# Performance work log

Measured on AMD Instinct MI355X. Metric: run time of the kernel, lower is better.

## Reference

```python
import jax, jax.numpy as jnp
import numpy as np

N_NODES = 100000
N_EDGES = 1600000
D = 128
L = 3


def setup_inputs() -> dict:
    key = jax.random.key(0)
    k1, k2, k3 = jax.random.split(key, 3)
    edge_index = jax.random.randint(k1, (2, N_EDGES), 0, N_NODES, dtype=jnp.int64)
    emb = jax.random.normal(k2, (N_NODES, D), dtype=jnp.float32)
    # Glorot-style scale for the per-layer linear weights
    Ws = jax.random.normal(k3, (L, D, D), dtype=jnp.float32) * (1.0 / np.sqrt(D))
    bs = jnp.zeros((L, D), dtype=jnp.float32)
    return {"edge_index": edge_index, "emb": emb, "Ws": Ws, "bs": bs}


def _gcn_forward(emb, Ws, bs, edge_index):
    n = emb.shape[0]
    self_loop = jnp.arange(n, dtype=edge_index.dtype)
    # PyG GCNConv adds self-loops and uses symmetric normalization
    row = jnp.concatenate([edge_index[0], self_loop])  # source nodes
    col = jnp.concatenate([edge_index[1], self_loop])  # target nodes
    deg = jax.ops.segment_sum(jnp.ones(row.shape[0], dtype=emb.dtype), col, num_segments=n)
    deg_inv_sqrt = jnp.where(deg > 0, jax.lax.rsqrt(jnp.maximum(deg, 1.0)), 0.0)
    norm = deg_inv_sqrt[row] * deg_inv_sqrt[col]  # [E+N]

    x = emb
    for l in range(Ws.shape[0]):
        h = x @ Ws[l]                              # [N, D] linear transform
        msg = h[row] * norm[:, None]               # gather + scale [E+N, D]
        x = jax.ops.segment_sum(msg, col, num_segments=n) + bs[l]  # scatter-add
        x = jax.nn.relu(x)                         # dropout is identity in eval
    return x


def reference(edge_index, emb, Ws, bs) -> jnp.ndarray:
    return _gcn_forward(emb, Ws, bs, edge_index)
```

## Files before the change

### kernel.cpp

```cpp
#include <hip/hip_runtime.h>
#include <hip/hip_fp16.h>
#include <cstdint>
#include <cstddef>

#define N_NODES 100000
#define N_EDGES 1600000
#define D 128
#define NLAYERS 3
#define NB 3125
#define NBLK_E 128
#define EPB 12500
#define ENT_CAP 1024

typedef __attribute__((ext_vector_type(8))) _Float16 half8;


__global__ __launch_bounds__(512) void hist1_kernel(const int* __restrict__ col,
                                                    int* __restrict__ hmat) {
    __shared__ int hist[NB];
    int b = blockIdx.x, t = threadIdx.x;
    for (int j = t; j < NB; j += 512) hist[j] = 0;
    __syncthreads();
    const int4* col4 = (const int4*)(col + b * EPB);
    for (int i = t; i < EPB / 4; i += 512) {
        int4 c = col4[i];
        atomicAdd(&hist[c.x >> 5], 1);
        atomicAdd(&hist[c.y >> 5], 1);
        atomicAdd(&hist[c.z >> 5], 1);
        atomicAdd(&hist[c.w >> 5], 1);
    }
    __syncthreads();
    for (int j = t; j < NB; j += 512) hmat[b * NB + j] = hist[j];
}

__global__ void btot_kernel(const int* __restrict__ hmat, int* __restrict__ btot) {
    int j = blockIdx.x * 256 + threadIdx.x;
    if (j < NB) {
        int s = 0;
        for (int b = 0; b < NBLK_E; b++) s += hmat[b * NB + j];
        btot[j] = s;
    }
}

__global__ void bscan_kernel(const int* __restrict__ btot, int* __restrict__ bstart, int nb, int e) {
    __shared__ int lsum[1024];
    int t = threadIdx.x;
    int vals[4];
    int v0 = 0;
#pragma unroll
    for (int j = 0; j < 4; j++) {
        int idx = t * 4 + j;
        int c = (idx < nb) ? btot[idx] : 0;
        vals[j] = c;
        v0 += c;
    }
    lsum[t] = v0;
    __syncthreads();
    for (int off = 1; off < 1024; off <<= 1) {
        int x = (t >= off) ? lsum[t - off] : 0;
        __syncthreads();
        lsum[t] += x;
        __syncthreads();
    }
    int base = lsum[t] - v0;
#pragma unroll
    for (int j = 0; j < 4; j++) {
        int idx = t * 4 + j;
        if (idx < nb) {
            bstart[idx] = base;
            base += vals[j];
        }
    }
    if (t == 0) bstart[nb] = e;
}

__global__ void hoff_kernel(const int* __restrict__ hmat, const int* __restrict__ bstart,
                            int* __restrict__ hoff) {
    int j = blockIdx.x * 256 + threadIdx.x;
    if (j < NB) {
        int run = bstart[j];
        for (int b = 0; b < NBLK_E; b++) {
            hoff[b * NB + j] = run;
            run += hmat[b * NB + j];
        }
    }
}

__global__ __launch_bounds__(512) void scatter_kernel(const int* __restrict__ row,
                                                      const int* __restrict__ col,
                                                      const int* __restrict__ hoff,
                                                      unsigned* __restrict__ bucketbuf) {
    __shared__ int cur[NB];
    int b = blockIdx.x, t = threadIdx.x;
    for (int j = t; j < NB; j += 512) cur[j] = hoff[b * NB + j];
    __syncthreads();
    int base = b * EPB;
    for (int i = t; i < EPB; i += 512) {
        int r = row[base + i], c = col[base + i];
        int pos = atomicAdd(&cur[c >> 5], 1);
        bucketbuf[pos] = ((unsigned)r << 5) | (unsigned)(c & 31);
    }
}

__global__ void fill2_kernel(const unsigned* __restrict__ bucketbuf, const int* __restrict__ bstart,
                             int* __restrict__ offsets, float* __restrict__ dinv,
                             int* __restrict__ src, int n, int e) {
    __shared__ unsigned ent[ENT_CAP];
    __shared__ int hist[32];
    __shared__ int cur[32];
    __shared__ int loff[32];
    int b = blockIdx.x, t = threadIdx.x;
    int s0 = bstart[b];
    int cnt = bstart[b + 1] - s0;
    if (cnt > ENT_CAP) cnt = ENT_CAP;
    if (t < 32) hist[t] = 0;
    __syncthreads();
    for (int i = t; i < cnt; i += 256) {
        unsigned v = bucketbuf[s0 + i];
        ent[i] = v;
        atomicAdd(&hist[v & 31], 1);
    }
    __syncthreads();
    if (t == 0) {
        int run = s0;
#pragma unroll
        for (int j = 0; j < 32; j++) {
            loff[j] = run;
            run += hist[j];
        }
    }
    __syncthreads();
    if (t < 32) {
        int node = b * 32 + t;
        int o = loff[t];
        offsets[node] = o;
        cur[t] = o;
        dinv[node] = rsqrtf((float)(hist[t] + 1));
    }
    if (b == 0 && t == 0) offsets[n] = e;
    __syncthreads();
    for (int i = t; i < cnt; i += 256) {
        unsigned v = ent[i];
        int pos = atomicAdd(&cur[v & 31], 1);
        src[pos] = (int)(v >> 5);
    }
}


__global__ void cast_kernel(const float2* __restrict__ in, const float* __restrict__ dinv,
                            __half2* __restrict__ out, int n2) {
    int i = blockIdx.x * 256 + threadIdx.x;
    if (i < n2) {
        float dv = dinv[i >> 6];
        float2 v = in[i];
        out[i] = __floats2half2_rn(dv * v.x, dv * v.y);
    }
}

__global__ __launch_bounds__(256) void agg_kernel(const __half* __restrict__ xs,
                                                  const int* __restrict__ offs,
                                                  const int* __restrict__ src,
                                                  const float* __restrict__ dinv,
                                                  float* __restrict__ out) {
    int wave = threadIdx.x >> 6;
    int lane = threadIdx.x & 63;
    int v = blockIdx.x * 4 + wave;
    int g = lane >> 4, f = lane & 15;
    const char* xb = (const char*)xs;

    float acc[8] = {0.f, 0.f, 0.f, 0.f, 0.f, 0.f, 0.f, 0.f};
    if (g == 0) {
        half8 hv = *(const half8*)(xb + ((size_t)v << 8) + (f << 4));
#pragma unroll
        for (int j = 0; j < 8; j++) acc[j] += (float)hv[j];
    }

    int o0 = offs[v], o1 = offs[v + 1];
    int i = o0 + g;
    for (; i + 4 < o1; i += 8) {
        int sA = src[i], sB = src[i + 4];
        half8 hA = *(const half8*)(xb + ((size_t)sA << 8) + (f << 4));
        half8 hB = *(const half8*)(xb + ((size_t)sB << 8) + (f << 4));
#pragma unroll
        for (int j = 0; j < 8; j++) acc[j] += (float)hA[j] + (float)hB[j];
    }
    if (i < o1) {
        int sA = src[i];
        half8 hA = *(const half8*)(xb + ((size_t)sA << 8) + (f << 4));
#pragma unroll
        for (int j = 0; j < 8; j++) acc[j] += (float)hA[j];
    }

#pragma unroll
    for (int j = 0; j < 8; j++) {
        acc[j] += __shfl_xor(acc[j], 16, 64);
        acc[j] += __shfl_xor(acc[j], 32, 64);
    }

    if (g < 2) {
        float dv = dinv[v];
        float4 w4;
        w4.x = dv * acc[g * 4 + 0];
        w4.y = dv * acc[g * 4 + 1];
        w4.z = dv * acc[g * 4 + 2];
        w4.w = dv * acc[g * 4 + 3];
        *(float4*)(out + (size_t)v * 128 + f * 8 + g * 4) = w4;
    }
}

__global__ __launch_bounds__(256, 2) void gemm_bias_relu_kernel(
    const float* __restrict__ A, const float* __restrict__ W,
    const float* __restrict__ bias, const float* __restrict__ dinv,
    float* __restrict__ out, __half2* __restrict__ xh_out, int write_h) {
    __shared__ float sW[128 * 128];
    __shared__ float sX[32 * 128];
    int t = threadIdx.x;
    int tx = t & 31;
    int ty = t >> 5;
    int row0 = blockIdx.x * 32;

    const float4* W4 = (const float4*)W;
    float4* sW4 = (float4*)sW;
#pragma unroll
    for (int i = 0; i < 16; i++) sW4[t + 256 * i] = W4[t + 256 * i];

    const float4* A4 = (const float4*)A;
    float4* sX4 = (float4*)sX;
#pragma unroll
    for (int i = 0; i < 4; i++) {
        int c = t + 256 * i;
        int r = c >> 5, kc = c & 31;
        sX4[r * 32 + kc] = A4[(size_t)(row0 + r) * 32 + kc];
    }
    __syncthreads();

    float4 acc[4];
#pragma unroll
    for (int r = 0; r < 4; r++) acc[r] = make_float4(0.f, 0.f, 0.f, 0.f);

#define FMA4(a, s, b) a.x += (s) * (b).x; a.y += (s) * (b).y; a.z += (s) * (b).z; a.w += (s) * (b).w;
#pragma unroll 4
    for (int k0 = 0; k0 < 128; k0 += 4) {
        float4 b0 = *(const float4*)&sW[(k0 + 0) * 128 + tx * 4];
        float4 b1 = *(const float4*)&sW[(k0 + 1) * 128 + tx * 4];
        float4 b2 = *(const float4*)&sW[(k0 + 2) * 128 + tx * 4];
        float4 b3 = *(const float4*)&sW[(k0 + 3) * 128 + tx * 4];
#pragma unroll
        for (int r = 0; r < 4; r++) {
            float4 a = *(const float4*)&sX[(ty * 4 + r) * 128 + k0];
            FMA4(acc[r], a.x, b0)
            FMA4(acc[r], a.y, b1)
            FMA4(acc[r], a.z, b2)
            FMA4(acc[r], a.w, b3)
        }
    }
#undef FMA4

    float4 bb = ((const float4*)bias)[tx];
#pragma unroll
    for (int r = 0; r < 4; r++) {
        float4 o;
        o.x = fmaxf(acc[r].x + bb.x, 0.0f);
        o.y = fmaxf(acc[r].y + bb.y, 0.0f);
        o.z = fmaxf(acc[r].z + bb.z, 0.0f);
        o.w = fmaxf(acc[r].w + bb.w, 0.0f);
        size_t rowi = (size_t)(row0 + ty * 4 + r);
        ((float4*)out)[rowi * 32 + tx] = o;
        if (write_h) {
            float dv = dinv[rowi];
            xh_out[rowi * 64 + tx * 2] = __floats2half2_rn(dv * o.x, dv * o.y);
            xh_out[rowi * 64 + tx * 2 + 1] = __floats2half2_rn(dv * o.z, dv * o.w);
        }
    }
}


extern "C" void kernel_launch(void* const* d_in, const int* in_sizes, int n_in,
                              void* d_out, int out_size, void* d_ws, size_t ws_size,
                              hipStream_t stream) {
    const int* edge = (const int*)d_in[0];
    const float* emb = (const float*)d_in[1];
    const float* Ws = (const float*)d_in[2];
    const float* bs = (const float*)d_in[3];
    float* out = (float*)d_out;

    const int n = N_NODES, e = N_EDGES;
    const int* row = edge;
    const int* col = edge + e;

    char* p = (char*)d_ws;
    float* aggbuf = (float*)p;
    int* hmat = (int*)p;
    int* hoff = hmat + (size_t)NBLK_E * NB;
    p += (size_t)n * D * 4;
    __half2* xh = (__half2*)p;
    unsigned* bucketbuf = (unsigned*)p;
    p += (size_t)n * D * 2;
    int* csr_src  = (int*)p;    p += (size_t)e * 4;
    float* dinv   = (float*)p;  p += (size_t)n * 4;
    int* offsets  = (int*)p;    p += (size_t)(n + 1) * 4;
    int* btot     = (int*)p;    p += (size_t)NB * 4;
    int* bstart   = (int*)p;    p += (size_t)(NB + 1) * 4;

    hist1_kernel<<<NBLK_E, 512, 0, stream>>>(col, hmat);
    btot_kernel<<<(NB + 255) / 256, 256, 0, stream>>>(hmat, btot);
    bscan_kernel<<<1, 1024, 0, stream>>>(btot, bstart, NB, e);
    hoff_kernel<<<(NB + 255) / 256, 256, 0, stream>>>(hmat, bstart, hoff);
    scatter_kernel<<<NBLK_E, 512, 0, stream>>>(row, col, hoff, bucketbuf);
    fill2_kernel<<<NB, 256, 0, stream>>>(bucketbuf, bstart, offsets, dinv, csr_src, n, e);

    int n2 = n * 64;
    cast_kernel<<<(n2 + 255) / 256, 256, 0, stream>>>((const float2*)emb, dinv, xh, n2);

    for (int l = 0; l < NLAYERS; l++) {
        agg_kernel<<<n / 4, 256, 0, stream>>>((const __half*)xh, offsets, csr_src, dinv, aggbuf);
        gemm_bias_relu_kernel<<<n / 32, 256, 0, stream>>>(
            aggbuf, Ws + (size_t)l * D * D, bs + (size_t)l * D, dinv, out,
            xh, (l < NLAYERS - 1) ? 1 : 0);
    }
}
```

Before: 544.1 us.

## Split half-precision features into eight column panels for cache-local aggregation

Stores the fp16 scaled features as 8 panels of 16 columns each ([panel][node][16]), so every aggregation block gathers from one 3.2 MB panel that can stay in L2/LLC instead of the full 25.6 MB matrix. The aggregation kernel now processes 32 nodes per block per panel, staging edge indices and offsets in shared memory, with 8 lanes per node each loading a half2. The cast and GEMM epilogue write the panel layout. The cost is 8x re-reading of the CSR index array and smaller 4-byte gathers per lane instead of 16-byte vectors.

```diff
diff --git a/kernel.cpp b/kernel.cpp
--- a/kernel.cpp
+++ b/kernel.cpp
@@ -11,8 +11,7 @@
 #define NBLK_E 128
 #define EPB 12500
 #define ENT_CAP 1024
-
-typedef __attribute__((ext_vector_type(8))) _Float16 half8;
+#define NPAN 8
 
 
 __global__ __launch_bounds__(512) void hist1_kernel(const int* __restrict__ col,
@@ -147,71 +146,77 @@
 }
 
 
-__global__ void cast_kernel(const float2* __restrict__ in, const float* __restrict__ dinv,
-                            __half2* __restrict__ out, int n2) {
+__global__ void cast_panel_kernel(const float2* __restrict__ in, const float* __restrict__ dinv,
+                                  __half2* __restrict__ xhp) {
     int i = blockIdx.x * 256 + threadIdx.x;
-    if (i < n2) {
-        float dv = dinv[i >> 6];
-        float2 v = in[i];
-        out[i] = __floats2half2_rn(dv * v.x, dv * v.y);
-    }
-}
-
-__global__ __launch_bounds__(256) void agg_kernel(const __half* __restrict__ xs,
-                                                  const int* __restrict__ offs,
-                                                  const int* __restrict__ src,
-                                                  const float* __restrict__ dinv,
-                                                  float* __restrict__ out) {
-    int wave = threadIdx.x >> 6;
-    int lane = threadIdx.x & 63;
-    int v = blockIdx.x * 4 + wave;
-    int g = lane >> 4, f = lane & 15;
-    const char* xb = (const char*)xs;
-
-    float acc[8] = {0.f, 0.f, 0.f, 0.f, 0.f, 0.f, 0.f, 0.f};
-    if (g == 0) {
-        half8 hv = *(const half8*)(xb + ((size_t)v << 8) + (f << 4));
-#pragma unroll
-        for (int j = 0; j < 8; j++) acc[j] += (float)hv[j];
-    }
-
-    int o0 = offs[v], o1 = offs[v + 1];
-    int i = o0 + g;
-    for (; i + 4 < o1; i += 8) {
-        int sA = src[i], sB = src[i + 4];
-        half8 hA = *(const half8*)(xb + ((size_t)sA << 8) + (f << 4));
-        half8 hB = *(const half8*)(xb + ((size_t)sB << 8) + (f << 4));
-#pragma unroll
-        for (int j = 0; j < 8; j++) acc[j] += (float)hA[j] + (float)hB[j];
-    }
-    if (i < o1) {
-        int sA = src[i];
-        half8 hA = *(const half8*)(xb + ((size_t)sA << 8) + (f << 4));
-#pragma unroll
-        for (int j = 0; j < 8; j++) acc[j] += (float)hA[j];
-    }
-
-#pragma unroll
-    for (int j = 0; j < 8; j++) {
-        acc[j] += __shfl_xor(acc[j], 16, 64);
-        acc[j] += __shfl_xor(acc[j], 32, 64);
-    }
-
-    if (g < 2) {
-        float dv = dinv[v];
-        float4 w4;
-        w4.x = dv * acc[g * 4 + 0];
-        w4.y = dv * acc[g * 4 + 1];
-        w4.z = dv * acc[g * 4 + 2];
-        w4.w = dv * acc[g * 4 + 3];
-        *(float4*)(out + (size_t)v * 128 + f * 8 + g * 4) = w4;
-    }
+    int p = blockIdx.y;
+    int v = i >> 3, f2 = i & 7;
+    float dv = dinv[v];
+    float2 val = in[(size_t)v * 64 + p * 8 + f2];
+    xhp[((size_t)p * N_NODES + v) * 8 + f2] = __floats2half2_rn(dv * val.x, dv * val.y);
+}
+
+__global__ __launch_bounds__(256) void agg_panel_kernel(const __half2* __restrict__ xhp,
+                                                        const int* __restrict__ offs,
+                                                        const int* __restrict__ src,
+                                                        const float* __restrict__ dinv,
+                                                        float* __restrict__ out) {
+    __shared__ int sedge[1024];
+    __shared__ int soff[33];
+    __shared__ float sdv[32];
+    int blk = blockIdx.x;
+    int p = blk & 7;
+    int v0 = (blk >> 3) * 32;
+    int t = threadIdx.x;
+    if (t < 33) soff[t] = offs[v0 + t];
+    if (t >= 64 && t < 96) sdv[t - 64] = dinv[v0 + (t - 64)];
+    __syncthreads();
+    int e0 = soff[0];
+    int cnt = soff[32] - e0;
+    int lim = cnt < 1024 ? cnt : 1024;
+    for (int i = t; i < lim; i += 256) sedge[i] = src[e0 + i];
+    __syncthreads();
+
+    int lane = t & 63;
+    int g = lane >> 3, f2 = lane & 7;
+    int vl = (t >> 6) * 8 + g;
+    int v = v0 + vl;
+    const __half2* xp = xhp + (size_t)p * (N_NODES * 8);
+
+    int o0 = soff[vl] - e0, o1 = soff[vl + 1] - e0;
+    float2 acc = __half22float2(xp[(size_t)v * 8 + f2]);
+
+    int iend = o1 < lim ? o1 : lim;
+    int i = o0;
+    for (; i + 1 < iend; i += 2) {
+        int sA = sedge[i], sB = sedge[i + 1];
+        float2 a = __half22float2(xp[(size_t)sA * 8 + f2]);
+        float2 b = __half22float2(xp[(size_t)sB * 8 + f2]);
+        acc.x += a.x + b.x;
+        acc.y += a.y + b.y;
+    }
+    if (i < iend) {
+        float2 a = __half22float2(xp[(size_t)sedge[i] * 8 + f2]);
+        acc.x += a.x;
+        acc.y += a.y;
+    }
+    for (int j = (o0 > lim ? o0 : lim); j < o1; j++) {
+        float2 a = __half22float2(xp[(size_t)src[e0 + j] * 8 + f2]);
+        acc.x += a.x;
+        acc.y += a.y;
+    }
+
+    float dv = sdv[vl];
+    float2 w;
+    w.x = dv * acc.x;
+    w.y = dv * acc.y;
+    ((float2*)out)[(size_t)v * 64 + p * 8 + f2] = w;
 }
 
 __global__ __launch_bounds__(256, 2) void gemm_bias_relu_kernel(
     const float* __restrict__ A, const float* __restrict__ W,
     const float* __restrict__ bias, const float* __restrict__ dinv,
-    float* __restrict__ out, __half2* __restrict__ xh_out, int write_h) {
+    float* __restrict__ out, __half2* __restrict__ xhp_out, int write_h) {
     __shared__ float sW[128 * 128];
     __shared__ float sX[32 * 128];
     int t = threadIdx.x;
@@ -268,8 +273,10 @@
         ((float4*)out)[rowi * 32 + tx] = o;
         if (write_h) {
             float dv = dinv[rowi];
-            xh_out[rowi * 64 + tx * 2] = __floats2half2_rn(dv * o.x, dv * o.y);
-            xh_out[rowi * 64 + tx * 2 + 1] = __floats2half2_rn(dv * o.z, dv * o.w);
+            int pp = tx >> 2;
+            size_t base = ((size_t)pp * N_NODES + rowi) * 8 + (tx & 3) * 2;
+            xhp_out[base] = __floats2half2_rn(dv * o.x, dv * o.y);
+            xhp_out[base + 1] = __floats2half2_rn(dv * o.z, dv * o.w);
         }
     }
 }
@@ -293,7 +300,7 @@
     int* hmat = (int*)p;
     int* hoff = hmat + (size_t)NBLK_E * NB;
     p += (size_t)n * D * 4;
-    __half2* xh = (__half2*)p;
+    __half2* xhp = (__half2*)p;
     unsigned* bucketbuf = (unsigned*)p;
     p += (size_t)n * D * 2;
     int* csr_src  = (int*)p;    p += (size_t)e * 4;
@@ -309,13 +316,13 @@
     scatter_kernel<<<NBLK_E, 512, 0, stream>>>(row, col, hoff, bucketbuf);
     fill2_kernel<<<NB, 256, 0, stream>>>(bucketbuf, bstart, offsets, dinv, csr_src, n, e);
 
-    int n2 = n * 64;
-    cast_kernel<<<(n2 + 255) / 256, 256, 0, stream>>>((const float2*)emb, dinv, xh, n2);
+    dim3 cgrid(n * 8 / 256, 8);
+    cast_panel_kernel<<<cgrid, 256, 0, stream>>>((const float2*)emb, dinv, xhp);
 
     for (int l = 0; l < NLAYERS; l++) {
-        agg_kernel<<<n / 4, 256, 0, stream>>>((const __half*)xh, offsets, csr_src, dinv, aggbuf);
+        agg_panel_kernel<<<(n / 32) * NPAN, 256, 0, stream>>>(xhp, offsets, csr_src, dinv, aggbuf);
         gemm_bias_relu_kernel<<<n / 32, 256, 0, stream>>>(
             aggbuf, Ws + (size_t)l * D * D, bs + (size_t)l * D, dinv, out,
-            xh, (l < NLAYERS - 1) ? 1 : 0);
-    }
-}
+            xhp, (l < NLAYERS - 1) ? 1 : 0);
+    }
+}
```

Measured after the change: 603.7 us. 1.11x slower.
